# Kernel tuning notes

Measured on AMD Instinct MI355X. Metric: run time of the kernel, lower is better.

## Reference

```python
import jax, jax.numpy as jnp
import numpy as np

B, S, HID = 2, 4096, 512
NH = 8
HD = HID // NH  # head dim 64


def setup_inputs() -> dict:
    key = jax.random.key(0)
    ks = jax.random.split(key, 9)
    scale = 1.0 / np.sqrt(HID)
    inp = {
        "query": jax.random.normal(ks[0], (B, S, HID), dtype=jnp.float32),
        "key": jax.random.normal(ks[1], (B, S, HID), dtype=jnp.float32),
        "value": jax.random.normal(ks[2], (B, S, HID), dtype=jnp.float32),
        "key_padding_mask": jnp.zeros((B, S), dtype=bool),
        "Wq": jax.random.normal(ks[3], (HID, HID), dtype=jnp.float32) * scale,
        "bq": jnp.zeros((HID,), dtype=jnp.float32),
        "Wk": jax.random.normal(ks[4], (HID, HID), dtype=jnp.float32) * scale,
        "bk": jnp.zeros((HID,), dtype=jnp.float32),
        "Wv": jax.random.normal(ks[5], (HID, HID), dtype=jnp.float32) * scale,
        "bv": jnp.zeros((HID,), dtype=jnp.float32),
    }
    return inp


def reference(query, key, value, key_padding_mask, Wq, bq, Wk, bk, Wv, bv):
    b, s, h = query.shape
    # projections (torch Linear: x @ W.T + b)
    q = query @ Wq.T + bq
    k = key @ Wk.T + bk
    v = value @ Wv.T + bv
    # split heads: [b, nh, s, hd]
    q = q.reshape(b, s, NH, HD).transpose(0, 2, 1, 3)
    k = k.reshape(b, s, NH, HD).transpose(0, 2, 1, 3)
    v = v.reshape(b, s, NH, HD).transpose(0, 2, 1, 3)
    scores = jnp.einsum("bnqd,bnkd->bnqk", q, k) / jnp.sqrt(jnp.float32(HD))
    scores = jnp.where(key_padding_mask[:, None, None, :], -jnp.inf, scores)
    weights = jax.nn.softmax(scores, axis=-1)  # dropout p=0.0 -> identity
    out = jnp.einsum("bnqk,bnkd->bnqd", weights, v)
    out = out.transpose(0, 2, 1, 3).reshape(b, s, h)
    return out, weights
```

## Files before the change

kernel.cpp:

```cpp
#include <hip/hip_runtime.h>

typedef __attribute__((ext_vector_type(4))) float f32x4;
typedef __attribute__((ext_vector_type(8))) short short8;
typedef __attribute__((ext_vector_type(8))) __bf16 bf16x8;
typedef __attribute__((ext_vector_type(4))) unsigned int u32x4;
typedef __attribute__((ext_vector_type(4))) unsigned short u16x4;
typedef unsigned short u16;
typedef unsigned int u32;

#define NB 2
#define S_LEN 4096
#define NHD 8
#define HID 512

__device__ __forceinline__ u16 f2bf(float f) {
  u32 u = __builtin_bit_cast(u32, f);
  u += 0x7fffu + ((u >> 16) & 1u);
  return (u16)(u >> 16);
}

template <typename V>
static __device__ __forceinline__ auto mfma_imp(V a, V b, f32x4 c, int)
    -> decltype(__builtin_amdgcn_mfma_f32_16x16x32_bf16(a, b, c, 0, 0, 0)) {
  return __builtin_amdgcn_mfma_f32_16x16x32_bf16(a, b, c, 0, 0, 0);
}
template <typename V>
static __device__ __forceinline__ f32x4 mfma_imp(V a, V b, f32x4 c, long) {
  return __builtin_amdgcn_mfma_f32_16x16x32_bf16(
      __builtin_bit_cast(bf16x8, a), __builtin_bit_cast(bf16x8, b), c, 0, 0, 0);
}
static __device__ __forceinline__ f32x4 mfma_bf16(short8 a, short8 b, f32x4 c) {
  return mfma_imp(a, b, c, 0);
}

#define WG_BARRIER()                                        \
  do {                                                      \
    asm volatile("s_waitcnt lgkmcnt(0)" ::: "memory");      \
    __builtin_amdgcn_sched_barrier(0);                      \
    __builtin_amdgcn_s_barrier();                           \
    __builtin_amdgcn_sched_barrier(0);                      \
  } while (0)

__global__ __launch_bounds__(256, 2) void proj_kernel(
    const float* __restrict__ Xq, const float* __restrict__ Xk,
    const float* __restrict__ Xv, const float* __restrict__ Wq,
    const float* __restrict__ Wk, const float* __restrict__ Wv,
    const float* __restrict__ bq_, const float* __restrict__ bk_,
    const float* __restrict__ bv_, u16* __restrict__ oq,
    u16* __restrict__ ok, u16* __restrict__ ov)
{
  __shared__ u16 Al[128 * 64];
  __shared__ u16 Bl[128 * 64];
  const int z = blockIdx.z;
  const float* X = (z == 0) ? Xq : (z == 1) ? Xk : Xv;
  const float* W = (z == 0) ? Wq : (z == 1) ? Wk : Wv;
  const float* bias = (z == 0) ? bq_ : (z == 1) ? bk_ : bv_;
  u16* out = (z == 0) ? oq : (z == 1) ? ok : ov;
  const int transposeOut = (z == 2);
  const float scale = (z == 0) ? 0.125f : 1.0f;

  const int tid = threadIdx.x;
  const int lane = tid & 63;
  const int wid = tid >> 6;
  const int wr = (wid >> 1) << 6;
  const int wc = (wid & 1) << 6;
  const int bm = blockIdx.x << 7;
  const int bn = blockIdx.y << 7;

  f32x4 acc[4][4] = {};

#pragma unroll 1
  for (int k0 = 0; k0 < HID; k0 += 64) {
    __syncthreads();
#pragma unroll
    for (int i = 0; i < 4; ++i) {
      const int idx = i * 256 + tid;
      const int row = idx >> 3;
      const int c = idx & 7;
      const int off = (row * 128 + c * 16) ^ ((row & 7) << 4);
      const float* ga = X + (size_t)(bm + row) * HID + k0 + c * 8;
      f32x4 a0 = *(const f32x4*)ga;
      f32x4 a1 = *(const f32x4*)(ga + 4);
      short8 pa;
      pa[0] = (short)f2bf(a0[0]); pa[1] = (short)f2bf(a0[1]);
      pa[2] = (short)f2bf(a0[2]); pa[3] = (short)f2bf(a0[3]);
      pa[4] = (short)f2bf(a1[0]); pa[5] = (short)f2bf(a1[1]);
      pa[6] = (short)f2bf(a1[2]); pa[7] = (short)f2bf(a1[3]);
      *(short8*)((char*)Al + off) = pa;
      const float* gb = W + (size_t)(bn + row) * HID + k0 + c * 8;
      f32x4 b0 = *(const f32x4*)gb;
      f32x4 b1 = *(const f32x4*)(gb + 4);
      short8 pb;
      pb[0] = (short)f2bf(b0[0]); pb[1] = (short)f2bf(b0[1]);
      pb[2] = (short)f2bf(b0[2]); pb[3] = (short)f2bf(b0[3]);
      pb[4] = (short)f2bf(b1[0]); pb[5] = (short)f2bf(b1[1]);
      pb[6] = (short)f2bf(b1[2]); pb[7] = (short)f2bf(b1[3]);
      *(short8*)((char*)Bl + off) = pb;
    }
    __syncthreads();
#pragma unroll
    for (int ks = 0; ks < 2; ++ks) {
      const int koffb = (ks * 32 + ((lane >> 4) << 3)) * 2;
      short8 af[4], bfr[4];
#pragma unroll
      for (int m = 0; m < 4; ++m) {
        const int row = wr + m * 16 + (lane & 15);
        af[m] = *(const short8*)((const char*)Al + ((row * 128 + koffb) ^ ((row & 7) << 4)));
      }
#pragma unroll
      for (int n = 0; n < 4; ++n) {
        const int row = wc + n * 16 + (lane & 15);
        bfr[n] = *(const short8*)((const char*)Bl + ((row * 128 + koffb) ^ ((row & 7) << 4)));
      }
#pragma unroll
      for (int m = 0; m < 4; ++m)
#pragma unroll
        for (int n = 0; n < 4; ++n)
          acc[m][n] = mfma_bf16(af[m], bfr[n], acc[m][n]);
    }
  }

#pragma unroll
  for (int n = 0; n < 4; ++n) {
    const int j = bn + wc + n * 16 + (lane & 15);
    const float bj = bias[j];
    const int h = j >> 6, d = j & 63;
#pragma unroll
    for (int m = 0; m < 4; ++m) {
      const int rbase = bm + wr + m * 16 + ((lane >> 4) << 2);
      const int b = rbase >> 12;
      const int s = rbase & (S_LEN - 1);
      if (!transposeOut) {
#pragma unroll
        for (int i = 0; i < 4; ++i) {
          const float v = (acc[m][n][i] + bj) * scale;
          out[(((size_t)(b * NHD + h) * S_LEN + (s + i)) << 6) + d] = f2bf(v);
        }
      } else {
        u16x4 pk;
#pragma unroll
        for (int i = 0; i < 4; ++i) pk[i] = f2bf((acc[m][n][i] + bj) * scale);
        *(u16x4*)(out + (((size_t)(b * NHD + h) * 64 + d) << 12) + s) = pk;
      }
    }
  }
}

__global__ __launch_bounds__(256, 2) void attn_kernel(
    const u16* __restrict__ Qp, const u16* __restrict__ Kp,
    const u16* __restrict__ Vt, const unsigned char* __restrict__ mask,
    float* __restrict__ outO, float* __restrict__ outW)
{
  __shared__ u16 Kl[128 * 64];
  __shared__ u16 Vl[64 * 128];
  __shared__ float Wl[4][16 * 128];
  __shared__ u32 anyMaskSh;

  const int tid = threadIdx.x;
  const int lane = tid & 63;
  const int wid = tid >> 6;
  const int lr = lane & 15;
  const int lg = lane >> 4;

  const int bid = blockIdx.x;
  const int swz = (bid & 7) * 64 + (bid >> 3);
  const int bh = swz >> 5;
  const int q0 = (swz & 31) << 7;
  const int b = bh >> 3;
  const int h = bh & 7;

  char* const Wlw = (char*)Wl[wid];

  int koff[4], kgo[4], voff[4], vgo[4];
#pragma unroll
  for (int i = 0; i < 4; ++i) {
    const int idx = i * 256 + tid;
    const int kr = idx >> 3, kc = idx & 7;
    koff[i] = (kr * 128 + kc * 16) ^ ((kr & 7) << 4);
    kgo[i] = (kr << 6) + kc * 8;
    const int vr = idx >> 4, vc = idx & 15;
    voff[i] = (vr * 256 + vc * 16) ^ ((vr & 7) << 4);
    vgo[i] = (vr << 12) + vc * 8;
  }
  const u16* kgbase = Kp + ((size_t)bh << 18);
  const u16* vgbase = Vt + ((size_t)bh << 18);

  if (tid == 0) anyMaskSh = 0u;
  __syncthreads();
  {
    u32x4 mv = *(const u32x4*)(mask + (size_t)b * S_LEN + tid * 16);
    if (mv[0] | mv[1] | mv[2] | mv[3]) atomicOr(&anyMaskSh, 1u);
  }
  __syncthreads();
  const bool anyMask = (anyMaskSh != 0u);

  short8 bq[2][2];
#pragma unroll
  for (int t = 0; t < 2; ++t)
#pragma unroll
    for (int ks = 0; ks < 2; ++ks) {
      const int qr = q0 + (t << 6) + (wid << 4) + lr;
      bq[t][ks] = *(const short8*)(
          Qp + (((size_t)bh * S_LEN + qr) << 6) + ks * 32 + lg * 8);
    }

  const unsigned char* mrow = mask + (size_t)b * S_LEN + (lg << 2);
  u32x4 rK[4], rV[4];

#pragma unroll
  for (int i = 0; i < 4; ++i) rK[i] = *(const u32x4*)(kgbase + kgo[i]);
#pragma unroll
  for (int i = 0; i < 4; ++i) *(u32x4*)((char*)Kl + koff[i]) = rK[i];
#pragma unroll
  for (int i = 0; i < 4; ++i) rK[i] = *(const u32x4*)(kgbase + (1 << 13) + kgo[i]);
  WG_BARRIER();

  float lsum0 = 0.f;
#pragma unroll 1
  for (int kt = 0; kt < 32; ++kt) {
#pragma unroll
    for (int rb = 0; rb < 8; ++rb) {
      const int krow = (rb << 4) + lr;
      short8 ak0 = *(const short8*)((const char*)Kl +
          ((krow * 128 + (lg << 4)) ^ ((krow & 7) << 4)));
      short8 ak1 = *(const short8*)((const char*)Kl +
          ((krow * 128 + 64 + (lg << 4)) ^ ((krow & 7) << 4)));
      u32 mw = 0u;
      if (anyMask) mw = *(const u32*)(mrow + (kt << 7) + (rb << 4));
      f32x4 sv = {};
      sv = mfma_bf16(ak0, bq[0][0], sv);
      sv = mfma_bf16(ak1, bq[0][1], sv);
      float p0 = __expf(sv[0]);
      float p1 = __expf(sv[1]);
      float p2 = __expf(sv[2]);
      float p3 = __expf(sv[3]);
      if (mw) {
        if (mw & 0x000000FFu) p0 = 0.f;
        if (mw & 0x0000FF00u) p1 = 0.f;
        if (mw & 0x00FF0000u) p2 = 0.f;
        if (mw & 0xFF000000u) p3 = 0.f;
      }
      lsum0 += (p0 + p1) + (p2 + p3);
    }
    WG_BARRIER();
    if (kt < 31) {
#pragma unroll
      for (int i = 0; i < 4; ++i) *(u32x4*)((char*)Kl + koff[i]) = rK[i];
    }
    if (kt < 30) {
#pragma unroll
      for (int i = 0; i < 4; ++i)
        rK[i] = *(const u32x4*)(kgbase + ((size_t)(kt + 2) << 13) + kgo[i]);
    }
    WG_BARRIER();
  }
  float inv0;
  {
    float t = lsum0;
    t += __shfl_xor(t, 16);
    t += __shfl_xor(t, 32);
    inv0 = 1.0f / t;
  }

#pragma unroll
  for (int i = 0; i < 4; ++i) {
    rK[i] = *(const u32x4*)(kgbase + kgo[i]);
    rV[i] = *(const u32x4*)(vgbase + vgo[i]);
  }
#pragma unroll
  for (int i = 0; i < 4; ++i) {
    *(u32x4*)((char*)Kl + koff[i]) = rK[i];
    *(u32x4*)((char*)Vl + voff[i]) = rV[i];
  }
#pragma unroll
  for (int i = 0; i < 4; ++i) {
    rK[i] = *(const u32x4*)(kgbase + (1 << 13) + kgo[i]);
    rV[i] = *(const u32x4*)(vgbase + (1 << 7) + vgo[i]);
  }
  WG_BARRIER();

  float lsum1 = 0.f;
  f32x4 oacc[4] = {};
  float* const wb0 = outW + ((size_t)(bh * S_LEN + q0 + (wid << 4)) << 12);
#pragma unroll 1
  for (int kt = 0; kt < 32; ++kt) {
#pragma unroll
    for (int rb = 0; rb < 8; ++rb) {
      const int krow = (rb << 4) + lr;
      short8 ak0 = *(const short8*)((const char*)Kl +
          ((krow * 128 + (lg << 4)) ^ ((krow & 7) << 4)));
      short8 ak1 = *(const short8*)((const char*)Kl +
          ((krow * 128 + 64 + (lg << 4)) ^ ((krow & 7) << 4)));
      u32 mw = 0u;
      if (anyMask) mw = *(const u32*)(mrow + (kt << 7) + (rb << 4));
      {
        f32x4 sv = {};
        sv = mfma_bf16(ak0, bq[0][0], sv);
        sv = mfma_bf16(ak1, bq[0][1], sv);
        float p0 = __expf(sv[0]) * inv0;
        float p1 = __expf(sv[1]) * inv0;
        float p2 = __expf(sv[2]) * inv0;
        float p3 = __expf(sv[3]) * inv0;
        if (mw) {
          if (mw & 0x000000FFu) p0 = 0.f;
          if (mw & 0x0000FF00u) p1 = 0.f;
          if (mw & 0x00FF0000u) p2 = 0.f;
          if (mw & 0xFF000000u) p3 = 0.f;
        }
        f32x4 wv; wv[0] = p0; wv[1] = p1; wv[2] = p2; wv[3] = p3;
        *(f32x4*)(Wlw + (((lr << 9) + (rb << 6) + (lg << 4)) ^ ((lr & 7) << 4))) = wv;
      }
      {
        f32x4 sv = {};
        sv = mfma_bf16(ak0, bq[1][0], sv);
        sv = mfma_bf16(ak1, bq[1][1], sv);
        float p0 = __expf(sv[0]);
        float p1 = __expf(sv[1]);
        float p2 = __expf(sv[2]);
        float p3 = __expf(sv[3]);
        if (mw) {
          if (mw & 0x000000FFu) p0 = 0.f;
          if (mw & 0x0000FF00u) p1 = 0.f;
          if (mw & 0x00FF0000u) p2 = 0.f;
          if (mw & 0xFF000000u) p3 = 0.f;
        }
        lsum1 += (p0 + p1) + (p2 + p3);
      }
    }
#pragma unroll
    for (int i = 0; i < 8; ++i) {
      const int row = (i << 1) + (lane >> 5);
      f32x4 wv = *(const f32x4*)(Wlw +
          (((row << 9) + ((lane & 31) << 4)) ^ ((row & 7) << 4)));
      __builtin_nontemporal_store(wv,
          (f32x4*)(wb0 + ((size_t)row << 12) + (kt << 7) + ((lane & 31) << 2)));
    }
#pragma unroll
    for (int kk = 0; kk < 4; ++kk) {
      const int wbo = (lr << 9) + (kk << 7) + (lg << 5);
      f32x4 a0 = *(const f32x4*)(Wlw + (wbo ^ ((lr & 7) << 4)));
      f32x4 a1 = *(const f32x4*)(Wlw + ((wbo + 16) ^ ((lr & 7) << 4)));
      short8 ap;
      ap[0] = (short)f2bf(a0[0]); ap[1] = (short)f2bf(a0[1]);
      ap[2] = (short)f2bf(a0[2]); ap[3] = (short)f2bf(a0[3]);
      ap[4] = (short)f2bf(a1[0]); ap[5] = (short)f2bf(a1[1]);
      ap[6] = (short)f2bf(a1[2]); ap[7] = (short)f2bf(a1[3]);
#pragma unroll
      for (int cd = 0; cd < 4; ++cd) {
        const int drow = (cd << 4) + lr;
        short8 bv = *(const short8*)((const char*)Vl +
            ((drow * 256 + (kk << 6) + (lg << 4)) ^ ((drow & 7) << 4)));
        oacc[cd] = mfma_bf16(ap, bv, oacc[cd]);
      }
    }
    WG_BARRIER();
    if (kt < 31) {
#pragma unroll
      for (int i = 0; i < 4; ++i) {
        *(u32x4*)((char*)Kl + koff[i]) = rK[i];
        *(u32x4*)((char*)Vl + voff[i]) = rV[i];
      }
    }
    if (kt < 30) {
#pragma unroll
      for (int i = 0; i < 4; ++i) {
        rK[i] = *(const u32x4*)(kgbase + ((size_t)(kt + 2) << 13) + kgo[i]);
        rV[i] = *(const u32x4*)(vgbase + ((size_t)(kt + 2) << 7) + vgo[i]);
      }
    }
    WG_BARRIER();
  }
  float inv1;
  {
    float t = lsum1;
    t += __shfl_xor(t, 16);
    t += __shfl_xor(t, 32);
    inv1 = 1.0f / t;
  }
#pragma unroll
  for (int cd = 0; cd < 4; ++cd)
#pragma unroll
    for (int i = 0; i < 4; ++i) {
      const int q = q0 + (wid << 4) + (lg << 2) + i;
      const int d = (cd << 4) + lr;
      __builtin_nontemporal_store(oacc[cd][i],
          outO + (((size_t)b * S_LEN + q) << 9) + h * 64 + d);
      oacc[cd][i] = 0.f;
    }

#pragma unroll
  for (int i = 0; i < 4; ++i) {
    rK[i] = *(const u32x4*)(kgbase + kgo[i]);
    rV[i] = *(const u32x4*)(vgbase + vgo[i]);
  }
#pragma unroll
  for (int i = 0; i < 4; ++i) {
    *(u32x4*)((char*)Kl + koff[i]) = rK[i];
    *(u32x4*)((char*)Vl + voff[i]) = rV[i];
  }
#pragma unroll
  for (int i = 0; i < 4; ++i) {
    rK[i] = *(const u32x4*)(kgbase + (1 << 13) + kgo[i]);
    rV[i] = *(const u32x4*)(vgbase + (1 << 7) + vgo[i]);
  }
  WG_BARRIER();

  float* const wb1 = outW + ((size_t)(bh * S_LEN + q0 + 64 + (wid << 4)) << 12);
#pragma unroll 1
  for (int kt = 0; kt < 32; ++kt) {
#pragma unroll
    for (int rb = 0; rb < 8; ++rb) {
      const int krow = (rb << 4) + lr;
      short8 ak0 = *(const short8*)((const char*)Kl +
          ((krow * 128 + (lg << 4)) ^ ((krow & 7) << 4)));
      short8 ak1 = *(const short8*)((const char*)Kl +
          ((krow * 128 + 64 + (lg << 4)) ^ ((krow & 7) << 4)));
      u32 mw = 0u;
      if (anyMask) mw = *(const u32*)(mrow + (kt << 7) + (rb << 4));
      f32x4 sv = {};
      sv = mfma_bf16(ak0, bq[1][0], sv);
      sv = mfma_bf16(ak1, bq[1][1], sv);
      float p0 = __expf(sv[0]) * inv1;
      float p1 = __expf(sv[1]) * inv1;
      float p2 = __expf(sv[2]) * inv1;
      float p3 = __expf(sv[3]) * inv1;
      if (mw) {
        if (mw & 0x000000FFu) p0 = 0.f;
        if (mw & 0x0000FF00u) p1 = 0.f;
        if (mw & 0x00FF0000u) p2 = 0.f;
        if (mw & 0xFF000000u) p3 = 0.f;
      }
      f32x4 wv; wv[0] = p0; wv[1] = p1; wv[2] = p2; wv[3] = p3;
      *(f32x4*)(Wlw + (((lr << 9) + (rb << 6) + (lg << 4)) ^ ((lr & 7) << 4))) = wv;
    }
#pragma unroll
    for (int i = 0; i < 8; ++i) {
      const int row = (i << 1) + (lane >> 5);
      f32x4 wv = *(const f32x4*)(Wlw +
          (((row << 9) + ((lane & 31) << 4)) ^ ((row & 7) << 4)));
      __builtin_nontemporal_store(wv,
          (f32x4*)(wb1 + ((size_t)row << 12) + (kt << 7) + ((lane & 31) << 2)));
    }
#pragma unroll
    for (int kk = 0; kk < 4; ++kk) {
      const int wbo = (lr << 9) + (kk << 7) + (lg << 5);
      f32x4 a0 = *(const f32x4*)(Wlw + (wbo ^ ((lr & 7) << 4)));
      f32x4 a1 = *(const f32x4*)(Wlw + ((wbo + 16) ^ ((lr & 7) << 4)));
      short8 ap;
      ap[0] = (short)f2bf(a0[0]); ap[1] = (short)f2bf(a0[1]);
      ap[2] = (short)f2bf(a0[2]); ap[3] = (short)f2bf(a0[3]);
      ap[4] = (short)f2bf(a1[0]); ap[5] = (short)f2bf(a1[1]);
      ap[6] = (short)f2bf(a1[2]); ap[7] = (short)f2bf(a1[3]);
#pragma unroll
      for (int cd = 0; cd < 4; ++cd) {
        const int drow = (cd << 4) + lr;
        short8 bv = *(const short8*)((const char*)Vl +
            ((drow * 256 + (kk << 6) + (lg << 4)) ^ ((drow & 7) << 4)));
        oacc[cd] = mfma_bf16(ap, bv, oacc[cd]);
      }
    }
    WG_BARRIER();
    if (kt < 31) {
#pragma unroll
      for (int i = 0; i < 4; ++i) {
        *(u32x4*)((char*)Kl + koff[i]) = rK[i];
        *(u32x4*)((char*)Vl + voff[i]) = rV[i];
      }
    }
    if (kt < 30) {
#pragma unroll
      for (int i = 0; i < 4; ++i) {
        rK[i] = *(const u32x4*)(kgbase + ((size_t)(kt + 2) << 13) + kgo[i]);
        rV[i] = *(const u32x4*)(vgbase + ((size_t)(kt + 2) << 7) + vgo[i]);
      }
    }
    WG_BARRIER();
  }
#pragma unroll
  for (int cd = 0; cd < 4; ++cd)
#pragma unroll
    for (int i = 0; i < 4; ++i) {
      const int q = q0 + 64 + (wid << 4) + (lg << 2) + i;
      const int d = (cd << 4) + lr;
      __builtin_nontemporal_store(oacc[cd][i],
          outO + (((size_t)b * S_LEN + q) << 9) + h * 64 + d);
    }
}

extern "C" void kernel_launch(void* const* d_in, const int* in_sizes, int n_in,
                              void* d_out, int out_size, void* d_ws, size_t ws_size,
                              hipStream_t stream) {
  (void)in_sizes; (void)n_in; (void)out_size; (void)ws_size;
  const float* query = (const float*)d_in[0];
  const float* key_i = (const float*)d_in[1];
  const float* value = (const float*)d_in[2];
  const unsigned char* kpm = (const unsigned char*)d_in[3];
  const float* Wq = (const float*)d_in[4];
  const float* bq_ = (const float*)d_in[5];
  const float* Wk = (const float*)d_in[6];
  const float* bk_ = (const float*)d_in[7];
  const float* Wv = (const float*)d_in[8];
  const float* bv_ = (const float*)d_in[9];

  u16* Qp = (u16*)d_ws;
  u16* Kp = Qp + (size_t)NB * NHD * S_LEN * 64;
  u16* Vt = Kp + (size_t)NB * NHD * S_LEN * 64;

  float* outO = (float*)d_out;
  float* outW = outO + (size_t)NB * S_LEN * HID;

  proj_kernel<<<dim3(64, 4, 3), dim3(256), 0, stream>>>(
      query, key_i, value, Wq, Wk, Wv, bq_, bk_, bv_, Qp, Kp, Vt);
  attn_kernel<<<dim3(512), dim3(256), 0, stream>>>(Qp, Kp, Vt, kpm, outO, outW);
}
```

Measured before the change: 307.2 us.

## Double-buffer K/V tiles in LDS and widen attention blocks to 8 waves

Doubles the workgroup to 512 threads (8 waves, 256 query rows per block) so each K/V tile loaded into LDS is shared by twice as many waves, and halves the grid to 256 blocks. K and V shared tiles become double-buffered, so the next tile is written while the current one is consumed, which removes one barrier per iteration. LDS use roughly doubles (about 128KB per block), so occupancy may drop to one block per CU. With only 256 blocks there may also be too few to fill the device.

New measurement: 337.2 us. +9.8%, slower.

```diff
diff --git a/kernel.cpp b/kernel.cpp
--- a/kernel.cpp
+++ b/kernel.cpp
@@ -146,14 +146,14 @@
   }
 }
 
-__global__ __launch_bounds__(256, 2) void attn_kernel(
+__global__ __launch_bounds__(512, 2) void attn_kernel(
     const u16* __restrict__ Qp, const u16* __restrict__ Kp,
     const u16* __restrict__ Vt, const unsigned char* __restrict__ mask,
     float* __restrict__ outO, float* __restrict__ outW)
 {
-  __shared__ u16 Kl[128 * 64];
-  __shared__ u16 Vl[64 * 128];
-  __shared__ float Wl[4][16 * 128];
+  __shared__ u16 Kl[2][128 * 64];
+  __shared__ u16 Vl[2][64 * 128];
+  __shared__ float Wl[8][16 * 128];
   __shared__ u32 anyMaskSh;
 
   const int tid = threadIdx.x;
@@ -163,18 +163,18 @@
   const int lg = lane >> 4;
 
   const int bid = blockIdx.x;
-  const int swz = (bid & 7) * 64 + (bid >> 3);
-  const int bh = swz >> 5;
-  const int q0 = (swz & 31) << 7;
+  const int swz = (bid & 7) * 32 + (bid >> 3);
+  const int bh = swz >> 4;
+  const int q0 = (swz & 15) << 8;
   const int b = bh >> 3;
   const int h = bh & 7;
 
   char* const Wlw = (char*)Wl[wid];
 
-  int koff[4], kgo[4], voff[4], vgo[4];
-#pragma unroll
-  for (int i = 0; i < 4; ++i) {
-    const int idx = i * 256 + tid;
+  int koff[2], kgo[2], voff[2], vgo[2];
+#pragma unroll
+  for (int i = 0; i < 2; ++i) {
+    const int idx = i * 512 + tid;
     const int kr = idx >> 3, kc = idx & 7;
     koff[i] = (kr * 128 + kc * 16) ^ ((kr & 7) << 4);
     kgo[i] = (kr << 6) + kc * 8;
@@ -187,7 +187,7 @@
 
   if (tid == 0) anyMaskSh = 0u;
   __syncthreads();
-  {
+  if (tid < 256) {
     u32x4 mv = *(const u32x4*)(mask + (size_t)b * S_LEN + tid * 16);
     if (mv[0] | mv[1] | mv[2] | mv[3]) atomicOr(&anyMaskSh, 1u);
   }
@@ -199,31 +199,42 @@
   for (int t = 0; t < 2; ++t)
 #pragma unroll
     for (int ks = 0; ks < 2; ++ks) {
-      const int qr = q0 + (t << 6) + (wid << 4) + lr;
+      const int qr = q0 + (t << 7) + (wid << 4) + lr;
       bq[t][ks] = *(const short8*)(
           Qp + (((size_t)bh * S_LEN + qr) << 6) + ks * 32 + lg * 8);
     }
 
   const unsigned char* mrow = mask + (size_t)b * S_LEN + (lg << 2);
-  u32x4 rK[4], rV[4];
-
-#pragma unroll
-  for (int i = 0; i < 4; ++i) rK[i] = *(const u32x4*)(kgbase + kgo[i]);
-#pragma unroll
-  for (int i = 0; i < 4; ++i) *(u32x4*)((char*)Kl + koff[i]) = rK[i];
-#pragma unroll
-  for (int i = 0; i < 4; ++i) rK[i] = *(const u32x4*)(kgbase + (1 << 13) + kgo[i]);
+  u32x4 rK[2], rV[2];
+
+#pragma unroll
+  for (int i = 0; i < 2; ++i) rK[i] = *(const u32x4*)(kgbase + kgo[i]);
+#pragma unroll
+  for (int i = 0; i < 2; ++i) *(u32x4*)((char*)Kl[0] + koff[i]) = rK[i];
+#pragma unroll
+  for (int i = 0; i < 2; ++i) rK[i] = *(const u32x4*)(kgbase + (1 << 13) + kgo[i]);
   WG_BARRIER();
 
   float lsum0 = 0.f;
 #pragma unroll 1
   for (int kt = 0; kt < 32; ++kt) {
+    const char* Kc = (const char*)Kl[kt & 1];
+    if (kt < 31) {
+#pragma unroll
+      for (int i = 0; i < 2; ++i)
+        *(u32x4*)((char*)Kl[(kt + 1) & 1] + koff[i]) = rK[i];
+    }
+    if (kt < 30) {
+#pragma unroll
+      for (int i = 0; i < 2; ++i)
+        rK[i] = *(const u32x4*)(kgbase + ((size_t)(kt + 2) << 13) + kgo[i]);
+    }
 #pragma unroll
     for (int rb = 0; rb < 8; ++rb) {
       const int krow = (rb << 4) + lr;
-      short8 ak0 = *(const short8*)((const char*)Kl +
+      short8 ak0 = *(const short8*)(Kc +
           ((krow * 128 + (lg << 4)) ^ ((krow & 7) << 4)));
-      short8 ak1 = *(const short8*)((const char*)Kl +
+      short8 ak1 = *(const short8*)(Kc +
           ((krow * 128 + 64 + (lg << 4)) ^ ((krow & 7) << 4)));
       u32 mw = 0u;
       if (anyMask) mw = *(const u32*)(mrow + (kt << 7) + (rb << 4));
@@ -243,16 +254,6 @@
       lsum0 += (p0 + p1) + (p2 + p3);
     }
     WG_BARRIER();
-    if (kt < 31) {
-#pragma unroll
-      for (int i = 0; i < 4; ++i) *(u32x4*)((char*)Kl + koff[i]) = rK[i];
-    }
-    if (kt < 30) {
-#pragma unroll
-      for (int i = 0; i < 4; ++i)
-        rK[i] = *(const u32x4*)(kgbase + ((size_t)(kt + 2) << 13) + kgo[i]);
-    }
-    WG_BARRIER();
   }
   float inv0;
   {
@@ -263,17 +264,17 @@
   }
 
 #pragma unroll
-  for (int i = 0; i < 4; ++i) {
+  for (int i = 0; i < 2; ++i) {
     rK[i] = *(const u32x4*)(kgbase + kgo[i]);
     rV[i] = *(const u32x4*)(vgbase + vgo[i]);
   }
 #pragma unroll
-  for (int i = 0; i < 4; ++i) {
-    *(u32x4*)((char*)Kl + koff[i]) = rK[i];
-    *(u32x4*)((char*)Vl + voff[i]) = rV[i];
-  }
-#pragma unroll
-  for (int i = 0; i < 4; ++i) {
+  for (int i = 0; i < 2; ++i) {
+    *(u32x4*)((char*)Kl[0] + koff[i]) = rK[i];
+    *(u32x4*)((char*)Vl[0] + voff[i]) = rV[i];
+  }
+#pragma unroll
+  for (int i = 0; i < 2; ++i) {
     rK[i] = *(const u32x4*)(kgbase + (1 << 13) + kgo[i]);
     rV[i] = *(const u32x4*)(vgbase + (1 << 7) + vgo[i]);
   }
@@ -284,12 +285,28 @@
   float* const wb0 = outW + ((size_t)(bh * S_LEN + q0 + (wid << 4)) << 12);
 #pragma unroll 1
   for (int kt = 0; kt < 32; ++kt) {
+    const char* Kc = (const char*)Kl[kt & 1];
+    const char* Vc = (const char*)Vl[kt & 1];
+    if (kt < 31) {
+#pragma unroll
+      for (int i = 0; i < 2; ++i) {
+        *(u32x4*)((char*)Kl[(kt + 1) & 1] + koff[i]) = rK[i];
+        *(u32x4*)((char*)Vl[(kt + 1) & 1] + voff[i]) = rV[i];
+      }
+    }
+    if (kt < 30) {
+#pragma unroll
+      for (int i = 0; i < 2; ++i) {
+        rK[i] = *(const u32x4*)(kgbase + ((size_t)(kt + 2) << 13) + kgo[i]);
+        rV[i] = *(const u32x4*)(vgbase + ((size_t)(kt + 2) << 7) + vgo[i]);
+      }
+    }
 #pragma unroll
     for (int rb = 0; rb < 8; ++rb) {
       const int krow = (rb << 4) + lr;
-      short8 ak0 = *(const short8*)((const char*)Kl +
+      short8 ak0 = *(const short8*)(Kc +
           ((krow * 128 + (lg << 4)) ^ ((krow & 7) << 4)));
-      short8 ak1 = *(const short8*)((const char*)Kl +
+      short8 ak1 = *(const short8*)(Kc +
           ((krow * 128 + 64 + (lg << 4)) ^ ((krow & 7) << 4)));
       u32 mw = 0u;
       if (anyMask) mw = *(const u32*)(mrow + (kt << 7) + (rb << 4));
@@ -348,24 +365,9 @@
 #pragma unroll
       for (int cd = 0; cd < 4; ++cd) {
         const int drow = (cd << 4) + lr;
-        short8 bv = *(const short8*)((const char*)Vl +
+        short8 bv = *(const short8*)(Vc +
             ((drow * 256 + (kk << 6) + (lg << 4)) ^ ((drow & 7) << 4)));
         oacc[cd] = mfma_bf16(ap, bv, oacc[cd]);
-      }
-    }
-    WG_BARRIER();
-    if (kt < 31) {
-#pragma unroll
-      for (int i = 0; i < 4; ++i) {
-        *(u32x4*)((char*)Kl + koff[i]) = rK[i];
-        *(u32x4*)((char*)Vl + voff[i]) = rV[i];
-      }
-    }
-    if (kt < 30) {
-#pragma unroll
-      for (int i = 0; i < 4; ++i) {
-        rK[i] = *(const u32x4*)(kgbase + ((size_t)(kt + 2) << 13) + kgo[i]);
-        rV[i] = *(const u32x4*)(vgbase + ((size_t)(kt + 2) << 7) + vgo[i]);
       }
     }
     WG_BARRIER();
@@ -389,31 +391,47 @@
     }
 
 #pragma unroll
-  for (int i = 0; i < 4; ++i) {
+  for (int i = 0; i < 2; ++i) {
     rK[i] = *(const u32x4*)(kgbase + kgo[i]);
     rV[i] = *(const u32x4*)(vgbase + vgo[i]);
   }
 #pragma unroll
-  for (int i = 0; i < 4; ++i) {
-    *(u32x4*)((char*)Kl + koff[i]) = rK[i];
-    *(u32x4*)((char*)Vl + voff[i]) = rV[i];
-  }
-#pragma unroll
-  for (int i = 0; i < 4; ++i) {
+  for (int i = 0; i < 2; ++i) {
+    *(u32x4*)((char*)Kl[0] + koff[i]) = rK[i];
+    *(u32x4*)((char*)Vl[0] + voff[i]) = rV[i];
+  }
+#pragma unroll
+  for (int i = 0; i < 2; ++i) {
     rK[i] = *(const u32x4*)(kgbase + (1 << 13) + kgo[i]);
     rV[i] = *(const u32x4*)(vgbase + (1 << 7) + vgo[i]);
   }
   WG_BARRIER();
 
-  float* const wb1 = outW + ((size_t)(bh * S_LEN + q0 + 64 + (wid << 4)) << 12);
+  float* const wb1 = outW + ((size_t)(bh * S_LEN + q0 + 128 + (wid << 4)) << 12);
 #pragma unroll 1
   for (int kt = 0; kt < 32; ++kt) {
+    const char* Kc = (const char*)Kl[kt & 1];
+    const char* Vc = (const char*)Vl[kt & 1];
+    if (kt < 31) {
+#pragma unroll
+      for (int i = 0; i < 2; ++i) {
+        *(u32x4*)((char*)Kl[(kt + 1) & 1] + koff[i]) = rK[i];
+        *(u32x4*)((char*)Vl[(kt + 1) & 1] + voff[i]) = rV[i];
+      }
+    }
+    if (kt < 30) {
+#pragma unroll
+      for (int i = 0; i < 2; ++i) {
+        rK[i] = *(const u32x4*)(kgbase + ((size_t)(kt + 2) << 13) + kgo[i]);
+        rV[i] = *(const u32x4*)(vgbase + ((size_t)(kt + 2) << 7) + vgo[i]);
+      }
+    }
 #pragma unroll
     for (int rb = 0; rb < 8; ++rb) {
       const int krow = (rb << 4) + lr;
-      short8 ak0 = *(const short8*)((const char*)Kl +
+      short8 ak0 = *(const short8*)(Kc +
           ((krow * 128 + (lg << 4)) ^ ((krow & 7) << 4)));
-      short8 ak1 = *(const short8*)((const char*)Kl +
+      short8 ak1 = *(const short8*)(Kc +
           ((krow * 128 + 64 + (lg << 4)) ^ ((krow & 7) << 4)));
       u32 mw = 0u;
       if (anyMask) mw = *(const u32*)(mrow + (kt << 7) + (rb << 4));
@@ -454,33 +472,18 @@
 #pragma unroll
       for (int cd = 0; cd < 4; ++cd) {
         const int drow = (cd << 4) + lr;
-        short8 bv = *(const short8*)((const char*)Vl +
+        short8 bv = *(const short8*)(Vc +
             ((drow * 256 + (kk << 6) + (lg << 4)) ^ ((drow & 7) << 4)));
         oacc[cd] = mfma_bf16(ap, bv, oacc[cd]);
       }
     }
     WG_BARRIER();
-    if (kt < 31) {
-#pragma unroll
-      for (int i = 0; i < 4; ++i) {
-        *(u32x4*)((char*)Kl + koff[i]) = rK[i];
-        *(u32x4*)((char*)Vl + voff[i]) = rV[i];
-      }
-    }
-    if (kt < 30) {
-#pragma unroll
-      for (int i = 0; i < 4; ++i) {
-        rK[i] = *(const u32x4*)(kgbase + ((size_t)(kt + 2) << 13) + kgo[i]);
-        rV[i] = *(const u32x4*)(vgbase + ((size_t)(kt + 2) << 7) + vgo[i]);
-      }
-    }
-    WG_BARRIER();
   }
 #pragma unroll
   for (int cd = 0; cd < 4; ++cd)
 #pragma unroll
     for (int i = 0; i < 4; ++i) {
-      const int q = q0 + 64 + (wid << 4) + (lg << 2) + i;
+      const int q = q0 + 128 + (wid << 4) + (lg << 2) + i;
       const int d = (cd << 4) + lr;
       __builtin_nontemporal_store(oacc[cd][i],
           outO + (((size_t)b * S_LEN + q) << 9) + h * 64 + d);
@@ -511,5 +514,5 @@
 
   proj_kernel<<<dim3(64, 4, 3), dim3(256), 0, stream>>>(
       query, key_i, value, Wq, Wk, Wv, bq_, bk_, bv_, Qp, Kp, Vt);
-  attn_kernel<<<dim3(512), dim3(256), 0, stream>>>(Qp, Kp, Vt, kpm, outO, outW);
-}
+  attn_kernel<<<dim3(256), dim3(512), 0, stream>>>(Qp, Kp, Vt, kpm, outO, outW);
+}
```

## Double-buffer K in LDS and stream V tiles directly into registers

Applied to the files above, without the earlier changes.

The K tile becomes a two-slot ring in shared memory. The next tile is written into the other slot at the start of each iteration, so every key loop needs only one workgroup barrier instead of two. V is no longer staged in LDS: each wave loads its MFMA B operands straight from global memory, and those loads are interleaved with the attention-weight stores to hide latency. This removes LDS traffic and barriers for V, but each of the four waves now fetches the same V data, which raises L2/global read traffic and register pressure.

Result: slower. 404.0 us (+31.5%).

```diff
diff --git a/kernel.cpp b/kernel.cpp
--- a/kernel.cpp
+++ b/kernel.cpp
@@ -151,8 +151,7 @@
     const u16* __restrict__ Vt, const unsigned char* __restrict__ mask,
     float* __restrict__ outO, float* __restrict__ outW)
 {
-  __shared__ u16 Kl[128 * 64];
-  __shared__ u16 Vl[64 * 128];
+  __shared__ u16 Kl[2][128 * 64];
   __shared__ float Wl[4][16 * 128];
   __shared__ u32 anyMaskSh;
 
@@ -171,19 +170,15 @@
 
   char* const Wlw = (char*)Wl[wid];
 
-  int koff[4], kgo[4], voff[4], vgo[4];
+  int koff[4], kgo[4];
 #pragma unroll
   for (int i = 0; i < 4; ++i) {
     const int idx = i * 256 + tid;
     const int kr = idx >> 3, kc = idx & 7;
     koff[i] = (kr * 128 + kc * 16) ^ ((kr & 7) << 4);
     kgo[i] = (kr << 6) + kc * 8;
-    const int vr = idx >> 4, vc = idx & 15;
-    voff[i] = (vr * 256 + vc * 16) ^ ((vr & 7) << 4);
-    vgo[i] = (vr << 12) + vc * 8;
   }
   const u16* kgbase = Kp + ((size_t)bh << 18);
-  const u16* vgbase = Vt + ((size_t)bh << 18);
 
   if (tid == 0) anyMaskSh = 0u;
   __syncthreads();
@@ -205,12 +200,16 @@
     }
 
   const unsigned char* mrow = mask + (size_t)b * S_LEN + (lg << 2);
-  u32x4 rK[4], rV[4];
+  u32x4 rK[4];
+
+#define VPTR(kt, kk, cd) ((const u32x4*)(Vt +                                  \
+    (((size_t)((bh << 6) + ((cd) << 4) + lr)) << 12) +                         \
+    ((kt) << 7) + ((kk) << 5) + (lg << 3)))
 
 #pragma unroll
   for (int i = 0; i < 4; ++i) rK[i] = *(const u32x4*)(kgbase + kgo[i]);
 #pragma unroll
-  for (int i = 0; i < 4; ++i) *(u32x4*)((char*)Kl + koff[i]) = rK[i];
+  for (int i = 0; i < 4; ++i) *(u32x4*)((char*)Kl[0] + koff[i]) = rK[i];
 #pragma unroll
   for (int i = 0; i < 4; ++i) rK[i] = *(const u32x4*)(kgbase + (1 << 13) + kgo[i]);
   WG_BARRIER();
@@ -218,12 +217,23 @@
   float lsum0 = 0.f;
 #pragma unroll 1
   for (int kt = 0; kt < 32; ++kt) {
+    const char* Kc = (const char*)Kl[kt & 1];
+    if (kt < 31) {
+#pragma unroll
+      for (int i = 0; i < 4; ++i)
+        *(u32x4*)((char*)Kl[(kt + 1) & 1] + koff[i]) = rK[i];
+    }
+    if (kt < 30) {
+#pragma unroll
+      for (int i = 0; i < 4; ++i)
+        rK[i] = *(const u32x4*)(kgbase + ((size_t)(kt + 2) << 13) + kgo[i]);
+    }
 #pragma unroll
     for (int rb = 0; rb < 8; ++rb) {
       const int krow = (rb << 4) + lr;
-      short8 ak0 = *(const short8*)((const char*)Kl +
+      short8 ak0 = *(const short8*)(Kc +
           ((krow * 128 + (lg << 4)) ^ ((krow & 7) << 4)));
-      short8 ak1 = *(const short8*)((const char*)Kl +
+      short8 ak1 = *(const short8*)(Kc +
           ((krow * 128 + 64 + (lg << 4)) ^ ((krow & 7) << 4)));
       u32 mw = 0u;
       if (anyMask) mw = *(const u32*)(mrow + (kt << 7) + (rb << 4));
@@ -243,16 +253,6 @@
       lsum0 += (p0 + p1) + (p2 + p3);
     }
     WG_BARRIER();
-    if (kt < 31) {
-#pragma unroll
-      for (int i = 0; i < 4; ++i) *(u32x4*)((char*)Kl + koff[i]) = rK[i];
-    }
-    if (kt < 30) {
-#pragma unroll
-      for (int i = 0; i < 4; ++i)
-        rK[i] = *(const u32x4*)(kgbase + ((size_t)(kt + 2) << 13) + kgo[i]);
-    }
-    WG_BARRIER();
   }
   float inv0;
   {
@@ -263,20 +263,11 @@
   }
 
 #pragma unroll
-  for (int i = 0; i < 4; ++i) {
-    rK[i] = *(const u32x4*)(kgbase + kgo[i]);
-    rV[i] = *(const u32x4*)(vgbase + vgo[i]);
-  }
-#pragma unroll
-  for (int i = 0; i < 4; ++i) {
-    *(u32x4*)((char*)Kl + koff[i]) = rK[i];
-    *(u32x4*)((char*)Vl + voff[i]) = rV[i];
-  }
-#pragma unroll
-  for (int i = 0; i < 4; ++i) {
-    rK[i] = *(const u32x4*)(kgbase + (1 << 13) + kgo[i]);
-    rV[i] = *(const u32x4*)(vgbase + (1 << 7) + vgo[i]);
-  }
+  for (int i = 0; i < 4; ++i) rK[i] = *(const u32x4*)(kgbase + kgo[i]);
+#pragma unroll
+  for (int i = 0; i < 4; ++i) *(u32x4*)((char*)Kl[0] + koff[i]) = rK[i];
+#pragma unroll
+  for (int i = 0; i < 4; ++i) rK[i] = *(const u32x4*)(kgbase + (1 << 13) + kgo[i]);
   WG_BARRIER();
 
   float lsum1 = 0.f;
@@ -284,12 +275,23 @@
   float* const wb0 = outW + ((size_t)(bh * S_LEN + q0 + (wid << 4)) << 12);
 #pragma unroll 1
   for (int kt = 0; kt < 32; ++kt) {
+    const char* Kc = (const char*)Kl[kt & 1];
+    if (kt < 31) {
+#pragma unroll
+      for (int i = 0; i < 4; ++i)
+        *(u32x4*)((char*)Kl[(kt + 1) & 1] + koff[i]) = rK[i];
+    }
+    if (kt < 30) {
+#pragma unroll
+      for (int i = 0; i < 4; ++i)
+        rK[i] = *(const u32x4*)(kgbase + ((size_t)(kt + 2) << 13) + kgo[i]);
+    }
 #pragma unroll
     for (int rb = 0; rb < 8; ++rb) {
       const int krow = (rb << 4) + lr;
-      short8 ak0 = *(const short8*)((const char*)Kl +
+      short8 ak0 = *(const short8*)(Kc +
           ((krow * 128 + (lg << 4)) ^ ((krow & 7) << 4)));
-      short8 ak1 = *(const short8*)((const char*)Kl +
+      short8 ak1 = *(const short8*)(Kc +
           ((krow * 128 + 64 + (lg << 4)) ^ ((krow & 7) << 4)));
       u32 mw = 0u;
       if (anyMask) mw = *(const u32*)(mrow + (kt << 7) + (rb << 4));
@@ -327,6 +329,11 @@
         lsum1 += (p0 + p1) + (p2 + p3);
       }
     }
+    u32x4 v0[4], v1[4], v2[4], v3[4];
+#pragma unroll
+    for (int cd = 0; cd < 4; ++cd) v0[cd] = *VPTR(kt, 0, cd);
+#pragma unroll
+    for (int cd = 0; cd < 4; ++cd) v1[cd] = *VPTR(kt, 1, cd);
 #pragma unroll
     for (int i = 0; i < 8; ++i) {
       const int row = (i << 1) + (lane >> 5);
@@ -335,6 +342,10 @@
       __builtin_nontemporal_store(wv,
           (f32x4*)(wb0 + ((size_t)row << 12) + (kt << 7) + ((lane & 31) << 2)));
     }
+#pragma unroll
+    for (int cd = 0; cd < 4; ++cd) v2[cd] = *VPTR(kt, 2, cd);
+#pragma unroll
+    for (int cd = 0; cd < 4; ++cd) v3[cd] = *VPTR(kt, 3, cd);
 #pragma unroll
     for (int kk = 0; kk < 4; ++kk) {
       const int wbo = (lr << 9) + (kk << 7) + (lg << 5);
@@ -345,28 +356,10 @@
       ap[2] = (short)f2bf(a0[2]); ap[3] = (short)f2bf(a0[3]);
       ap[4] = (short)f2bf(a1[0]); ap[5] = (short)f2bf(a1[1]);
       ap[6] = (short)f2bf(a1[2]); ap[7] = (short)f2bf(a1[3]);
-#pragma unroll
-      for (int cd = 0; cd < 4; ++cd) {
-        const int drow = (cd << 4) + lr;
-        short8 bv = *(const short8*)((const char*)Vl +
-            ((drow * 256 + (kk << 6) + (lg << 4)) ^ ((drow & 7) << 4)));
-        oacc[cd] = mfma_bf16(ap, bv, oacc[cd]);
-      }
-    }
-    WG_BARRIER();
-    if (kt < 31) {
-#pragma unroll
-      for (int i = 0; i < 4; ++i) {
-        *(u32x4*)((char*)Kl + koff[i]) = rK[i];
-        *(u32x4*)((char*)Vl + voff[i]) = rV[i];
-      }
-    }
-    if (kt < 30) {
-#pragma unroll
-      for (int i = 0; i < 4; ++i) {
-        rK[i] = *(const u32x4*)(kgbase + ((size_t)(kt + 2) << 13) + kgo[i]);
-        rV[i] = *(const u32x4*)(vgbase + ((size_t)(kt + 2) << 7) + vgo[i]);
-      }
+      const u32x4* vg = (kk == 0) ? v0 : (kk == 1) ? v1 : (kk == 2) ? v2 : v3;
+#pragma unroll
+      for (int cd = 0; cd < 4; ++cd)
+        oacc[cd] = mfma_bf16(ap, __builtin_bit_cast(short8, vg[cd]), oacc[cd]);
     }
     WG_BARRIER();
   }
@@ -389,31 +382,33 @@
     }
 
 #pragma unroll
-  for (int i = 0; i < 4; ++i) {
-    rK[i] = *(const u32x4*)(kgbase + kgo[i]);
-    rV[i] = *(const u32x4*)(vgbase + vgo[i]);
-  }
-#pragma unroll
-  for (int i = 0; i < 4; ++i) {
-    *(u32x4*)((char*)Kl + koff[i]) = rK[i];
-    *(u32x4*)((char*)Vl + voff[i]) = rV[i];
-  }
-#pragma unroll
-  for (int i = 0; i < 4; ++i) {
-    rK[i] = *(const u32x4*)(kgbase + (1 << 13) + kgo[i]);
-    rV[i] = *(const u32x4*)(vgbase + (1 << 7) + vgo[i]);
-  }
+  for (int i = 0; i < 4; ++i) rK[i] = *(const u32x4*)(kgbase + kgo[i]);
+#pragma unroll
+  for (int i = 0; i < 4; ++i) *(u32x4*)((char*)Kl[0] + koff[i]) = rK[i];
+#pragma unroll
+  for (int i = 0; i < 4; ++i) rK[i] = *(const u32x4*)(kgbase + (1 << 13) + kgo[i]);
   WG_BARRIER();
 
   float* const wb1 = outW + ((size_t)(bh * S_LEN + q0 + 64 + (wid << 4)) << 12);
 #pragma unroll 1
   for (int kt = 0; kt < 32; ++kt) {
+    const char* Kc = (const char*)Kl[kt & 1];
+    if (kt < 31) {
+#pragma unroll
+      for (int i = 0; i < 4; ++i)
+        *(u32x4*)((char*)Kl[(kt + 1) & 1] + koff[i]) = rK[i];
+    }
+    if (kt < 30) {
+#pragma unroll
+      for (int i = 0; i < 4; ++i)
+        rK[i] = *(const u32x4*)(kgbase + ((size_t)(kt + 2) << 13) + kgo[i]);
+    }
 #pragma unroll
     for (int rb = 0; rb < 8; ++rb) {
       const int krow = (rb << 4) + lr;
-      short8 ak0 = *(const short8*)((const char*)Kl +
+      short8 ak0 = *(const short8*)(Kc +
           ((krow * 128 + (lg << 4)) ^ ((krow & 7) << 4)));
-      short8 ak1 = *(const short8*)((const char*)Kl +
+      short8 ak1 = *(const short8*)(Kc +
           ((krow * 128 + 64 + (lg << 4)) ^ ((krow & 7) << 4)));
       u32 mw = 0u;
       if (anyMask) mw = *(const u32*)(mrow + (kt << 7) + (rb << 4));
@@ -433,6 +428,11 @@
       f32x4 wv; wv[0] = p0; wv[1] = p1; wv[2] = p2; wv[3] = p3;
       *(f32x4*)(Wlw + (((lr << 9) + (rb << 6) + (lg << 4)) ^ ((lr & 7) << 4))) = wv;
     }
+    u32x4 v0[4], v1[4], v2[4], v3[4];
+#pragma unroll
+    for (int cd = 0; cd < 4; ++cd) v0[cd] = *VPTR(kt, 0, cd);
+#pragma unroll
+    for (int cd = 0; cd < 4; ++cd) v1[cd] = *VPTR(kt, 1, cd);
 #pragma unroll
     for (int i = 0; i < 8; ++i) {
       const int row = (i << 1) + (lane >> 5);
@@ -441,6 +441,10 @@
       __builtin_nontemporal_store(wv,
           (f32x4*)(wb1 + ((size_t)row << 12) + (kt << 7) + ((lane & 31) << 2)));
     }
+#pragma unroll
+    for (int cd = 0; cd < 4; ++cd) v2[cd] = *VPTR(kt, 2, cd);
+#pragma unroll
+    for (int cd = 0; cd < 4; ++cd) v3[cd] = *VPTR(kt, 3, cd);
 #pragma unroll
     for (int kk = 0; kk < 4; ++kk) {
       const int wbo = (lr << 9) + (kk << 7) + (lg << 5);
@@ -451,28 +455,10 @@
       ap[2] = (short)f2bf(a0[2]); ap[3] = (short)f2bf(a0[3]);
       ap[4] = (short)f2bf(a1[0]); ap[5] = (short)f2bf(a1[1]);
       ap[6] = (short)f2bf(a1[2]); ap[7] = (short)f2bf(a1[3]);
-#pragma unroll
-      for (int cd = 0; cd < 4; ++cd) {
-        const int drow = (cd << 4) + lr;
-        short8 bv = *(const short8*)((const char*)Vl +
-            ((drow * 256 + (kk << 6) + (lg << 4)) ^ ((drow & 7) << 4)));
-        oacc[cd] = mfma_bf16(ap, bv, oacc[cd]);
-      }
-    }
-    WG_BARRIER();
-    if (kt < 31) {
-#pragma unroll
-      for (int i = 0; i < 4; ++i) {
-        *(u32x4*)((char*)Kl + koff[i]) = rK[i];
-        *(u32x4*)((char*)Vl + voff[i]) = rV[i];
-      }
-    }
-    if (kt < 30) {
-#pragma unroll
-      for (int i = 0; i < 4; ++i) {
-        rK[i] = *(const u32x4*)(kgbase + ((size_t)(kt + 2) << 13) + kgo[i]);
-        rV[i] = *(const u32x4*)(vgbase + ((size_t)(kt + 2) << 7) + vgo[i]);
-      }
+      const u32x4* vg = (kk == 0) ? v0 : (kk == 1) ? v1 : (kk == 2) ? v2 : v3;
+#pragma unroll
+      for (int cd = 0; cd < 4; ++cd)
+        oacc[cd] = mfma_bf16(ap, __builtin_bit_cast(short8, vg[cd]), oacc[cd]);
     }
     WG_BARRIER();
   }
@@ -485,6 +471,7 @@
       __builtin_nontemporal_store(oacc[cd][i],
           outO + (((size_t)b * S_LEN + q) << 9) + h * 64 + d);
     }
+#undef VPTR
 }
 
 extern "C" void kernel_launch(void* const* d_in, const int* in_sizes, int n_in,
```
